# Kernel tuning notes

Measured on AMD Instinct MI355X. Metric: run time of the kernel, lower is better.

The kernel has to match this reference:

```python
import jax, jax.numpy as jnp
import numpy as np

NT, C, B, N, H, E = 32768, 128, 64, 512, 4, 524288  # total nodes, channels, graphs, nodes/graph, heads, edges
DH = C // H
EPS = 1e-5


def batchnorm(x, g, b):
    # BatchNorm1d over the node dimension (training-mode batch statistics)
    m = x.mean(axis=0)
    v = x.var(axis=0)
    return (x - m) * jax.lax.rsqrt(v + EPS) * g + b


def setup_inputs() -> dict:
    key = jax.random.key(0)
    ks = jax.random.split(key, 8)
    s = 1.0 / np.sqrt(C)
    return dict(
        x=jax.random.normal(ks[0], (NT, C), jnp.float32),
        edge_index=jax.random.randint(ks[1], (2, E), 0, NT, dtype=jnp.int32),
        Wc=jax.random.normal(ks[2], (C, C), jnp.float32) * s,
        bc=jnp.zeros((C,), jnp.float32),
        in_proj_w=jax.random.normal(ks[3], (3 * C, C), jnp.float32) * s,
        in_proj_b=jnp.zeros((3 * C,), jnp.float32),
        out_proj_w=jax.random.normal(ks[4], (C, C), jnp.float32) * s,
        out_proj_b=jnp.zeros((C,), jnp.float32),
        gn1=jnp.ones((C,), jnp.float32), bn1=jnp.zeros((C,), jnp.float32),
        gn2=jnp.ones((C,), jnp.float32), bn2=jnp.zeros((C,), jnp.float32),
        gn3=jnp.ones((C,), jnp.float32), bn3=jnp.zeros((C,), jnp.float32),
        Wm1=jax.random.normal(ks[5], (2 * C, C), jnp.float32) * s,
        bm1=jnp.zeros((2 * C,), jnp.float32),
        Wm2=jax.random.normal(ks[6], (C, 2 * C), jnp.float32) / np.sqrt(2 * C),
        bm2=jnp.zeros((C,), jnp.float32),
    )


def reference(x, edge_index, Wc, bc, in_proj_w, in_proj_b, out_proj_w, out_proj_b,
              gn1, bn1, gn2, bn2, gn3, bn3, Wm1, bm1, Wm2, bm2):
    # --- local branch: mean-aggregation message passing + linear + residual + BN ---
    src, dst = edge_index[0], edge_index[1]
    agg = jax.ops.segment_sum(x[src], dst, num_segments=NT)            # [NT, C]
    cnt = jax.ops.segment_sum(jnp.ones((E, 1), x.dtype), dst, num_segments=NT)
    agg = agg / jnp.maximum(cnt, 1.0)
    h_local = agg @ Wc.T + bc + x                                       # dropout p=0 -> no-op
    h_local = batchnorm(h_local, gn1, bn1)

    # --- global branch: to_dense_batch (equal-size graphs -> reshape) + MHA ---
    hd = x.reshape(B, N, C)
    qkv = hd @ in_proj_w.T + in_proj_b                                  # [B, N, 3C]
    q, k, v = jnp.split(qkv, 3, axis=-1)
    q = q.reshape(B, N, H, DH).transpose(0, 2, 1, 3)                    # [B, H, N, DH]
    k = k.reshape(B, N, H, DH).transpose(0, 2, 1, 3)
    v = v.reshape(B, N, H, DH).transpose(0, 2, 1, 3)
    scores = jnp.einsum('bhqd,bhkd->bhqk', q, k) / np.sqrt(DH)          # [B, H, N, N]
    attn = jax.nn.softmax(scores, axis=-1)
    o = jnp.einsum('bhqk,bhkd->bhqd', attn, v)                          # [B, H, N, DH]
    o = o.transpose(0, 2, 1, 3).reshape(B, N, C)
    h_attn = (o @ out_proj_w.T + out_proj_b).reshape(NT, C) + x
    h_attn = batchnorm(h_attn, gn2, bn2)

    # --- combine + MLP + final norm ---
    out = h_local + h_attn
    out = out + (jax.nn.relu(out @ Wm1.T + bm1) @ Wm2.T + bm2)
    return batchnorm(out, gn3, bn3)
```

## Files before the change

### kernel.cpp

```cpp
#include <hip/hip_runtime.h>
#include <cstddef>

#define NT    32768
#define CCH   128
#define BB    64
#define NNODE 512
#define NHEAD 4
#define DHEAD 32
#define EE    524288
#define EPS   1e-5f
#define MAXDEG 96
#define CURPAD 16
#define SSLOT  8
#define EGRP  2048

typedef unsigned short u16;
typedef unsigned int   u32;
typedef __attribute__((ext_vector_type(8))) short short8;
typedef __attribute__((ext_vector_type(4))) short short4v;
typedef __attribute__((ext_vector_type(4))) float f32x4;

__device__ __forceinline__ float b2f(u32 w) { return __uint_as_float(w << 16); }
__device__ __forceinline__ u16 f2b(float f) {
    u32 u = __float_as_uint(f);
    u += 0x7FFF + ((u >> 16) & 1);
    return (u16)(u >> 16);
}

__global__ __launch_bounds__(256) void prep_kernel(const float* __restrict__ x,
                                                   const float* __restrict__ Wc,
                                                   const float* __restrict__ Wqkv,
                                                   const float* __restrict__ Wo,
                                                   const float* __restrict__ Wm1,
                                                   const float* __restrict__ Wm2,
                                                   u16* __restrict__ xb,
                                                   u16* __restrict__ Wcb,
                                                   u16* __restrict__ Wqkvb,
                                                   u16* __restrict__ Wob,
                                                   u16* __restrict__ Wm1b,
                                                   u16* __restrict__ Wm2b,
                                                   const int* __restrict__ ei,
                                                   int* __restrict__ cursor,
                                                   int* __restrict__ bucket) {
    if (blockIdx.x >= 2120) {
        int b2 = blockIdx.x - 2120;
        int k = b2 & 7;
        int g = b2 >> 3;
        int base_e = g * EGRP;
        for (int j = threadIdx.x; j < EGRP; j += 256) {
            int dst = ei[EE + base_e + j];
            if ((dst & 7) == k) {
                int src = ei[base_e + j];
                int pos = atomicAdd(cursor + dst * CURPAD, 1);
                if (pos < MAXDEG) bucket[dst * MAXDEG + pos] = src;
            }
        }
        return;
    }
    int r = blockIdx.x * 256 + threadIdx.x;
    const float* src; u16* dst;
    if (r < 524288) { src = x; dst = xb; }
    else if ((r -= 524288) < 2048) { src = Wc; dst = Wcb; }
    else if ((r -= 2048) < 6144) { src = Wqkv; dst = Wqkvb; }
    else if ((r -= 6144) < 2048) { src = Wo; dst = Wob; }
    else if ((r -= 2048) < 4096) { src = Wm1; dst = Wm1b; }
    else { r -= 4096; src = Wm2; dst = Wm2b; }
    size_t base = (size_t)r * 8;
    float4 a = *(const float4*)(src + base);
    float4 b = *(const float4*)(src + base + 4);
    uint4 u;
    u.x = (u32)f2b(a.x) | ((u32)f2b(a.y) << 16);
    u.y = (u32)f2b(a.z) | ((u32)f2b(a.w) << 16);
    u.z = (u32)f2b(b.x) | ((u32)f2b(b.y) << 16);
    u.w = (u32)f2b(b.z) | ((u32)f2b(b.w) << 16);
    *(uint4*)(dst + base) = u;
}

__global__ __launch_bounds__(256) void aggregate(const int* __restrict__ bucket,
                                                 const int* __restrict__ cursor,
                                                 const u16* __restrict__ xb,
                                                 u16* __restrict__ agg) {
    __shared__ int srcs[16][MAXDEG];
    int ln = threadIdx.x >> 4;
    int c8 = threadIdx.x & 15;
    int n = blockIdx.x * 16 + ln;
    int d = min(cursor[n * CURPAD], MAXDEG);
    for (int j = c8; j < d; j += 16) srcs[ln][j] = bucket[n * MAXDEG + j];
    __syncthreads();
    const u16* xp = xb + c8 * 8;
    float s[8] = {0.f, 0.f, 0.f, 0.f, 0.f, 0.f, 0.f, 0.f};
    for (int base = 0; base < d; base += 8) {
        uint4 w[8];
#pragma unroll
        for (int u = 0; u < 8; ++u) {
            int jj = base + u;
            int idx = srcs[ln][jj < d ? jj : 0];
            w[u] = *(const uint4*)(xp + (size_t)idx * CCH);
        }
#pragma unroll
        for (int u = 0; u < 8; ++u) {
            if (base + u >= d) { w[u].x = 0; w[u].y = 0; w[u].z = 0; w[u].w = 0; }
            s[0] += b2f(w[u].x & 0xffffu);
            s[1] += b2f(w[u].x >> 16);
            s[2] += b2f(w[u].y & 0xffffu);
            s[3] += b2f(w[u].y >> 16);
            s[4] += b2f(w[u].z & 0xffffu);
            s[5] += b2f(w[u].z >> 16);
            s[6] += b2f(w[u].w & 0xffffu);
            s[7] += b2f(w[u].w >> 16);
        }
    }
    float inv = 1.0f / fmaxf((float)d, 1.0f);
    uint4 out;
    out.x = (u32)f2b(s[0] * inv) | ((u32)f2b(s[1] * inv) << 16);
    out.y = (u32)f2b(s[2] * inv) | ((u32)f2b(s[3] * inv) << 16);
    out.z = (u32)f2b(s[4] * inv) | ((u32)f2b(s[5] * inv) << 16);
    out.w = (u32)f2b(s[6] * inv) | ((u32)f2b(s[7] * inv) << 16);
    *(uint4*)(agg + (size_t)n * CCH + c8 * 8) = out;
}

struct GemmSmem {
    u16 As[128 * 32];
    u16 Bs[128 * 32];
    u16 Cs[4][16 * 72];
    float csum[128];
    float csq[128];
};

template <bool RELU, int RESID, bool STATS>
__device__ __forceinline__ void gemm_body(GemmSmem& sm,
                                          const u16* __restrict__ A,
                                          const u16* __restrict__ W,
                                          const float* __restrict__ bias,
                                          const u16* __restrict__ residb,
                                          u16* __restrict__ outb, int ostride,
                                          float* __restrict__ sum, float* __restrict__ sumsq,
                                          int slotbase, int m0, int K) {
    int tid = threadIdx.x;
    int lane = tid & 63, wave = tid >> 6;
    int wm = (wave & 1) * 64, wn = (wave >> 1) * 64;
    int l15 = lane & 15, l4 = lane >> 4;

    if (STATS) {
        if (tid < 128) { sm.csum[tid] = 0.f; sm.csq[tid] = 0.f; }
    }

    f32x4 zero = {0.f, 0.f, 0.f, 0.f};
    f32x4 acc[4][4];
#pragma unroll
    for (int i = 0; i < 4; ++i)
#pragma unroll
        for (int j = 0; j < 4; ++j) acc[i][j] = zero;

    int srow = tid >> 2;
    int scol = (tid & 3) * 8;

    int kIter = K >> 5;
    uint4 a0 = *(const uint4*)(A + (size_t)(m0 + srow) * K + scol);
    uint4 a1 = *(const uint4*)(A + (size_t)(m0 + srow + 64) * K + scol);
    uint4 b0 = *(const uint4*)(W + (size_t)srow * K + scol);
    uint4 b1 = *(const uint4*)(W + (size_t)(srow + 64) * K + scol);
    for (int ki = 0; ki < kIter; ++ki) {
        if (ki) __syncthreads();
        *(uint4*)&sm.As[srow * 32 + scol] = a0;
        *(uint4*)&sm.As[(srow + 64) * 32 + scol] = a1;
        *(uint4*)&sm.Bs[srow * 32 + scol] = b0;
        *(uint4*)&sm.Bs[(srow + 64) * 32 + scol] = b1;
        if (ki + 1 < kIter) {
            int k0 = (ki + 1) * 32;
            a0 = *(const uint4*)(A + (size_t)(m0 + srow) * K + k0 + scol);
            a1 = *(const uint4*)(A + (size_t)(m0 + srow + 64) * K + k0 + scol);
            b0 = *(const uint4*)(W + (size_t)srow * K + k0 + scol);
            b1 = *(const uint4*)(W + (size_t)(srow + 64) * K + k0 + scol);
        }
        __syncthreads();
        short8 af[4], bf[4];
#pragma unroll
        for (int t = 0; t < 4; ++t) {
            af[t] = *(const short8*)&sm.As[(wm + t * 16 + l15) * 32 + l4 * 8];
            bf[t] = *(const short8*)&sm.Bs[(wn + t * 16 + l15) * 32 + l4 * 8];
        }
#pragma unroll
        for (int mt = 0; mt < 4; ++mt)
#pragma unroll
            for (int nt = 0; nt < 4; ++nt)
                acc[mt][nt] = __builtin_amdgcn_mfma_f32_16x16x32_bf16(af[mt], bf[nt], acc[mt][nt], 0, 0, 0);
    }

    float ps[4] = {0.f, 0.f, 0.f, 0.f};
    float pq[4] = {0.f, 0.f, 0.f, 0.f};
    int rl = lane >> 3;
    int cg = lane & 7;
#pragma unroll
    for (int mt = 0; mt < 4; ++mt) {
#pragma unroll
        for (int nt = 0; nt < 4; ++nt) {
            int lcol = wn + nt * 16 + l15;
            float bs = bias[lcol];
#pragma unroll
            for (int r = 0; r < 4; ++r) {
                int row = m0 + wm + mt * 16 + l4 * 4 + r;
                float v = acc[mt][nt][r] + bs;
                if (RESID == 2) v += b2f(residb[(size_t)row * 128 + lcol]);
                if (RELU) v = fmaxf(v, 0.0f);
                sm.Cs[wave][(l4 * 4 + r) * 72 + nt * 16 + l15] = f2b(v);
                if (STATS) { ps[nt] += v; pq[nt] += v * v; }
            }
        }
#pragma unroll
        for (int p = 0; p < 2; ++p) {
            int lrow = p * 8 + rl;
            uint4 wv = *(const uint4*)&sm.Cs[wave][lrow * 72 + cg * 8];
            int grow = m0 + wm + mt * 16 + lrow;
            *(uint4*)(outb + (size_t)grow * ostride + wn + cg * 8) = wv;
        }
    }
    if (STATS) {
#pragma unroll
        for (int nt = 0; nt < 4; ++nt) {
            atomicAdd(&sm.csum[wn + nt * 16 + l15], ps[nt]);
            atomicAdd(&sm.csq[wn + nt * 16 + l15], pq[nt]);
        }
        __syncthreads();
        if (tid < 128) {
            atomicAdd(sum + slotbase + tid, sm.csum[tid]);
            atomicAdd(sumsq + slotbase + tid, sm.csq[tid]);
        }
    }
}

__global__ __launch_bounds__(256) void gemm_wc_qkv(const u16* __restrict__ aggb,
                                                   const u16* __restrict__ Wcb,
                                                   const float* __restrict__ bc,
                                                   const u16* __restrict__ xb,
                                                   u16* __restrict__ hlocb,
                                                   float* __restrict__ sum1,
                                                   float* __restrict__ sq1,
                                                   const u16* __restrict__ Wqkvb,
                                                   const float* __restrict__ bqkv,
                                                   u16* __restrict__ qkvb) {
    __shared__ GemmSmem sm;
    int y = blockIdx.y;
    int m0 = blockIdx.x * 128;
    if (y == 0) {
        gemm_body<false, 2, true>(sm, aggb, Wcb, bc, xb, hlocb, 128, sum1, sq1,
                                  (blockIdx.x & (SSLOT - 1)) << 7, m0, 128);
    } else {
        gemm_body<false, 0, false>(sm, xb, Wqkvb + (size_t)(y - 1) * 16384,
                                   bqkv + (y - 1) * 128, nullptr,
                                   qkvb + (y - 1) * 128, 384, nullptr, nullptr, 0, m0, 128);
    }
}

__global__ __launch_bounds__(256) void gemm_wo(const u16* __restrict__ ob,
                                               const u16* __restrict__ Wob,
                                               const float* __restrict__ bo,
                                               const u16* __restrict__ xb,
                                               u16* __restrict__ t2b,
                                               float* __restrict__ sum2, float* __restrict__ sq2) {
    __shared__ GemmSmem sm;
    gemm_body<false, 2, true>(sm, ob, Wob, bo, xb, t2b, 128, sum2, sq2,
                              (blockIdx.x & (SSLOT - 1)) << 7, blockIdx.x * 128, 128);
}

__global__ __launch_bounds__(256) void gemm_mlp2(const u16* __restrict__ hidb,
                                                 const u16* __restrict__ Wm2b,
                                                 const float* __restrict__ bm2,
                                                 const u16* __restrict__ shb,
                                                 u16* __restrict__ out2b,
                                                 float* __restrict__ sum3, float* __restrict__ sq3) {
    __shared__ GemmSmem sm;
    gemm_body<false, 2, true>(sm, hidb, Wm2b, bm2, shb, out2b, 128, sum3, sq3,
                              (blockIdx.x & (SSLOT - 1)) << 7, blockIdx.x * 128, 256);
}

__global__ __launch_bounds__(256) void gemm_m1c(const u16* __restrict__ hlocb,
                                                const u16* __restrict__ t2b,
                                                const float* __restrict__ sum1,
                                                const float* __restrict__ sq1,
                                                const float* __restrict__ g1,
                                                const float* __restrict__ bt1,
                                                const float* __restrict__ sum2,
                                                const float* __restrict__ sq2,
                                                const float* __restrict__ g2,
                                                const float* __restrict__ bt2,
                                                u16* __restrict__ shb,
                                                const u16* __restrict__ Wm1b,
                                                const float* __restrict__ bm1,
                                                u16* __restrict__ hidb) {
    __shared__ u16 As[128 * 32];
    __shared__ u16 Bs[128 * 32];
    __shared__ u16 Cs[4][16 * 72];
    __shared__ float AF1[128], BF1[128], AF2[128], BF2[128];
    int tid = threadIdx.x;
    {
        int c = tid & 127;
        const float* sm = (tid < 128) ? sum1 : sum2;
        const float* sq = (tid < 128) ? sq1 : sq2;
        const float* g  = (tid < 128) ? g1 : g2;
        const float* bt = (tid < 128) ? bt1 : bt2;
        float s = 0.f, q = 0.f;
#pragma unroll
        for (int sl = 0; sl < SSLOT; ++sl) { s += sm[sl * 128 + c]; q += sq[sl * 128 + c]; }
        float m = s * (1.0f / NT);
        float v = q * (1.0f / NT) - m * m;
        float a = g[c] * rsqrtf(v + EPS);
        if (tid < 128) { AF1[c] = a; BF1[c] = bt[c] - m * a; }
        else           { AF2[c] = a; BF2[c] = bt[c] - m * a; }
    }
    int m0 = blockIdx.x * 128, n0 = blockIdx.y * 128;
    int lane = tid & 63, wave = tid >> 6;
    int wm = (wave & 1) * 64, wn = (wave >> 1) * 64;
    int l15 = lane & 15, l4 = lane >> 4;

    f32x4 zero = {0.f, 0.f, 0.f, 0.f};
    f32x4 acc[4][4];
#pragma unroll
    for (int i = 0; i < 4; ++i)
#pragma unroll
        for (int j = 0; j < 4; ++j) acc[i][j] = zero;

    int srow = tid >> 2;
    int scol = (tid & 3) * 8;
    bool wr = (blockIdx.y == 0);

    uint4 h0 = *(const uint4*)(hlocb + (size_t)(m0 + srow) * 128 + scol);
    uint4 h1 = *(const uint4*)(hlocb + (size_t)(m0 + srow + 64) * 128 + scol);
    uint4 t0 = *(const uint4*)(t2b + (size_t)(m0 + srow) * 128 + scol);
    uint4 t1 = *(const uint4*)(t2b + (size_t)(m0 + srow + 64) * 128 + scol);
    uint4 b0 = *(const uint4*)(Wm1b + (size_t)(n0 + srow) * 128 + scol);
    uint4 b1 = *(const uint4*)(Wm1b + (size_t)(n0 + srow + 64) * 128 + scol);
    __syncthreads();
    for (int ki = 0; ki < 4; ++ki) {
        int k0 = ki * 32;
        if (ki) __syncthreads();
        uint4 c0, c1;
        {
            const u32 hw[4] = {h0.x, h0.y, h0.z, h0.w};
            const u32 tw[4] = {t0.x, t0.y, t0.z, t0.w};
            u32 ow[4];
#pragma unroll
            for (int p = 0; p < 4; ++p) {
                int cc = k0 + scol + p * 2;
                float v0 = AF1[cc] * b2f(hw[p] & 0xffffu) + BF1[cc] + AF2[cc] * b2f(tw[p] & 0xffffu) + BF2[cc];
                float v1 = AF1[cc + 1] * b2f(hw[p] >> 16) + BF1[cc + 1] + AF2[cc + 1] * b2f(tw[p] >> 16) + BF2[cc + 1];
                ow[p] = (u32)f2b(v0) | ((u32)f2b(v1) << 16);
            }
            c0.x = ow[0]; c0.y = ow[1]; c0.z = ow[2]; c0.w = ow[3];
        }
        {
            const u32 hw[4] = {h1.x, h1.y, h1.z, h1.w};
            const u32 tw[4] = {t1.x, t1.y, t1.z, t1.w};
            u32 ow[4];
#pragma unroll
            for (int p = 0; p < 4; ++p) {
                int cc = k0 + scol + p * 2;
                float v0 = AF1[cc] * b2f(hw[p] & 0xffffu) + BF1[cc] + AF2[cc] * b2f(tw[p] & 0xffffu) + BF2[cc];
                float v1 = AF1[cc + 1] * b2f(hw[p] >> 16) + BF1[cc + 1] + AF2[cc + 1] * b2f(tw[p] >> 16) + BF2[cc + 1];
                ow[p] = (u32)f2b(v0) | ((u32)f2b(v1) << 16);
            }
            c1.x = ow[0]; c1.y = ow[1]; c1.z = ow[2]; c1.w = ow[3];
        }
        *(uint4*)&As[srow * 32 + scol] = c0;
        *(uint4*)&As[(srow + 64) * 32 + scol] = c1;
        *(uint4*)&Bs[srow * 32 + scol] = b0;
        *(uint4*)&Bs[(srow + 64) * 32 + scol] = b1;
        if (wr) {
            *(uint4*)(shb + (size_t)(m0 + srow) * 128 + k0 + scol) = c0;
            *(uint4*)(shb + (size_t)(m0 + srow + 64) * 128 + k0 + scol) = c1;
        }
        if (ki < 3) {
            int kn = k0 + 32;
            h0 = *(const uint4*)(hlocb + (size_t)(m0 + srow) * 128 + kn + scol);
            h1 = *(const uint4*)(hlocb + (size_t)(m0 + srow + 64) * 128 + kn + scol);
            t0 = *(const uint4*)(t2b + (size_t)(m0 + srow) * 128 + kn + scol);
            t1 = *(const uint4*)(t2b + (size_t)(m0 + srow + 64) * 128 + kn + scol);
            b0 = *(const uint4*)(Wm1b + (size_t)(n0 + srow) * 128 + kn + scol);
            b1 = *(const uint4*)(Wm1b + (size_t)(n0 + srow + 64) * 128 + kn + scol);
        }
        __syncthreads();
        short8 af[4], bf[4];
#pragma unroll
        for (int t = 0; t < 4; ++t) {
            af[t] = *(const short8*)&As[(wm + t * 16 + l15) * 32 + l4 * 8];
            bf[t] = *(const short8*)&Bs[(wn + t * 16 + l15) * 32 + l4 * 8];
        }
#pragma unroll
        for (int mt = 0; mt < 4; ++mt)
#pragma unroll
            for (int nt = 0; nt < 4; ++nt)
                acc[mt][nt] = __builtin_amdgcn_mfma_f32_16x16x32_bf16(af[mt], bf[nt], acc[mt][nt], 0, 0, 0);
    }

    int rl = lane >> 3;
    int cg = lane & 7;
#pragma unroll
    for (int mt = 0; mt < 4; ++mt) {
#pragma unroll
        for (int nt = 0; nt < 4; ++nt) {
            int col = n0 + wn + nt * 16 + l15;
            float bs = bm1[col];
#pragma unroll
            for (int r = 0; r < 4; ++r) {
                float v = fmaxf(acc[mt][nt][r] + bs, 0.0f);
                Cs[wave][(l4 * 4 + r) * 72 + nt * 16 + l15] = f2b(v);
            }
        }
#pragma unroll
        for (int p = 0; p < 2; ++p) {
            int lrow = p * 8 + rl;
            uint4 wv = *(const uint4*)&Cs[wave][lrow * 72 + cg * 8];
            int grow = m0 + wm + mt * 16 + lrow;
            *(uint4*)(hidb + (size_t)grow * 256 + n0 + wn + cg * 8) = wv;
        }
    }
}

__global__ __launch_bounds__(256) void final_bn(const u16* __restrict__ X,
                                                const float* __restrict__ sum3,
                                                const float* __restrict__ sq3,
                                                const float* __restrict__ g3,
                                                const float* __restrict__ bt3,
                                                float* __restrict__ outp) {
    __shared__ float A3[128], B3[128];
    int t = threadIdx.x;
    if (t < 128) {
        float s = 0.f, q = 0.f;
#pragma unroll
        for (int sl = 0; sl < SSLOT; ++sl) { s += sum3[sl * 128 + t]; q += sq3[sl * 128 + t]; }
        float m = s * (1.0f / NT);
        float v = q * (1.0f / NT) - m * m;
        float a = g3[t] * rsqrtf(v + EPS);
        A3[t] = a;
        B3[t] = bt3[t] - m * a;
    }
    __syncthreads();
    int i8 = blockIdx.x * 256 + t;
    size_t i = (size_t)i8 * 8;
    int c = (int)(i & (CCH - 1));
    uint4 u = *(const uint4*)(X + i);
    float x[8];
    x[0] = b2f(u.x & 0xffffu); x[1] = b2f(u.x >> 16);
    x[2] = b2f(u.y & 0xffffu); x[3] = b2f(u.y >> 16);
    x[4] = b2f(u.z & 0xffffu); x[5] = b2f(u.z >> 16);
    x[6] = b2f(u.w & 0xffffu); x[7] = b2f(u.w >> 16);
    float4 o0, o1;
    o0.x = A3[c + 0] * x[0] + B3[c + 0];
    o0.y = A3[c + 1] * x[1] + B3[c + 1];
    o0.z = A3[c + 2] * x[2] + B3[c + 2];
    o0.w = A3[c + 3] * x[3] + B3[c + 3];
    o1.x = A3[c + 4] * x[4] + B3[c + 4];
    o1.y = A3[c + 5] * x[5] + B3[c + 5];
    o1.z = A3[c + 6] * x[6] + B3[c + 6];
    o1.w = A3[c + 7] * x[7] + B3[c + 7];
    *(float4*)(outp + i) = o0;
    *(float4*)(outp + i + 4) = o1;
}

__global__ __launch_bounds__(512) void attn_mfma(const u16* __restrict__ qkv,
                                                 u16* __restrict__ o) {
    __shared__ __align__(16) u16 Ks[512 * 40];
    __shared__ __align__(16) u16 Vt[32 * 520];
    int bh = blockIdx.x;
    int b = bh >> 2, h = bh & 3;
    int tid = threadIdx.x;
    int lane = tid & 63, wave = tid >> 6;
    int quad = lane >> 4, l15 = lane & 15;
    const float scale = 0.1767766952966369f;

    const u16* kvbase = qkv + (size_t)b * 512 * 384 + 128 + h * 32;
    for (int idx = tid; idx < 2048; idx += 512) {
        int row = idx >> 2, c = idx & 3;
        *(uint4*)&Ks[row * 40 + c * 8] = *(const uint4*)(kvbase + (size_t)row * 384 + c * 8);
    }
    for (int idx = tid; idx < 2048; idx += 512) {
        int row = idx >> 2, c = idx & 3;
        uint4 u = *(const uint4*)(kvbase + 128 + (size_t)row * 384 + c * 8);
        u16 e[8];
        *(uint4*)e = u;
#pragma unroll
        for (int i = 0; i < 8; ++i) Vt[(c * 8 + i) * 520 + row] = e[i];
    }
    __syncthreads();

    f32x4 zero = {0.f, 0.f, 0.f, 0.f};
    for (int qt = 0; qt < 4; ++qt) {
        int qbase = wave * 64 + qt * 16;
        short8 qf = *(const short8*)(qkv + (size_t)(b * 512 + qbase + l15) * 384 + h * 32 + quad * 8);
        float lq = 0.f;
        f32x4 oa[2] = {zero, zero};

        for (int kv0 = 0; kv0 < 512; kv0 += 64) {
            f32x4 s[4];
#pragma unroll
            for (int t = 0; t < 4; ++t) {
                short8 kb = *(const short8*)&Ks[(kv0 + t * 16 + l15) * 40 + quad * 8];
                s[t] = __builtin_amdgcn_mfma_f32_16x16x32_bf16(kb, qf, zero, 0, 0, 0);
            }
            short8 pp[2];
#pragma unroll
            for (int t = 0; t < 4; ++t) {
                float p0 = __expf(s[t][0] * scale);
                float p1 = __expf(s[t][1] * scale);
                float p2 = __expf(s[t][2] * scale);
                float p3 = __expf(s[t][3] * scale);
                lq += (p0 + p1) + (p2 + p3);
                int hi = (t & 1) * 4;
                pp[t >> 1][hi + 0] = (short)f2b(p0);
                pp[t >> 1][hi + 1] = (short)f2b(p1);
                pp[t >> 1][hi + 2] = (short)f2b(p2);
                pp[t >> 1][hi + 3] = (short)f2b(p3);
            }
#pragma unroll
            for (int tp = 0; tp < 2; ++tp) {
                int tb = kv0 + tp * 32;
#pragma unroll
                for (int n = 0; n < 2; ++n) {
                    const u16* vrow = &Vt[(n * 16 + l15) * 520 + tb + quad * 4];
                    short4v va = *(const short4v*)vrow;
                    short4v vb2 = *(const short4v*)(vrow + 16);
                    short8 vv = {va.x, va.y, va.z, va.w, vb2.x, vb2.y, vb2.z, vb2.w};
                    oa[n] = __builtin_amdgcn_mfma_f32_16x16x32_bf16(pp[tp], vv, oa[n], 0, 0, 0);
                }
            }
        }
        lq += __shfl_xor(lq, 16);
        lq += __shfl_xor(lq, 32);
        u16* op = o + (size_t)(b * 512 + qbase) * 128 + h * 32;
#pragma unroll
        for (int r = 0; r < 4; ++r) {
            float Lr = __shfl(lq, quad * 4 + r);
            float inv = 1.0f / Lr;
#pragma unroll
            for (int n = 0; n < 2; ++n)
                op[(quad * 4 + r) * 128 + n * 16 + l15] = f2b(oa[n][r] * inv);
        }
    }
}

extern "C" void kernel_launch(void* const* d_in, const int* in_sizes, int n_in,
                              void* d_out, int out_size, void* d_ws, size_t ws_size,
                              hipStream_t stream) {
    const float* x    = (const float*)d_in[0];
    const int*   ei   = (const int*)d_in[1];
    const float* Wc   = (const float*)d_in[2];
    const float* bc   = (const float*)d_in[3];
    const float* Wqkv = (const float*)d_in[4];
    const float* bqkv = (const float*)d_in[5];
    const float* Wo   = (const float*)d_in[6];
    const float* bo   = (const float*)d_in[7];
    const float* gn1  = (const float*)d_in[8];
    const float* bn1b = (const float*)d_in[9];
    const float* gn2  = (const float*)d_in[10];
    const float* bn2b = (const float*)d_in[11];
    const float* gn3  = (const float*)d_in[12];
    const float* bn3b = (const float*)d_in[13];
    const float* Wm1  = (const float*)d_in[14];
    const float* bm1  = (const float*)d_in[15];
    const float* Wm2  = (const float*)d_in[16];
    const float* bm2  = (const float*)d_in[17];
    float* outp = (float*)d_out;

    char* w = (char*)d_ws;
    const size_t MB = 1024 * 1024;
    u16* xb    = (u16*)(w);
    u16* hlocb = (u16*)(w + 8 * MB);
    u16* t2b   = (u16*)(w + 16 * MB);
    u16* out2b = (u16*)(w + 24 * MB);
    u16* qkvb  = (u16*)(w + 32 * MB);
    u16* hidb  = (u16*)(w + 56 * MB);
    u16* shb   = (u16*)(w + 72 * MB);
    int* bucket = (int*)(w + 80 * MB);
    int* cursor = (int*)(w + 92 * MB);
    float* stats = (float*)(w + 94 * MB);
    u16* Wcb   = (u16*)(w + 95 * MB);
    u16* Wqkvb = Wcb + 16384;
    u16* Wob   = Wqkvb + 49152;
    u16* Wm1b  = Wob + 16384;
    u16* Wm2b  = Wm1b + 32768;
    u16* ob    = (u16*)(w + 96 * MB);
    float* sum1 = stats;                  float* sq1 = stats + 1024;
    float* sum2 = stats + 2048;           float* sq2 = stats + 3072;
    float* sum3 = stats + 4096;           float* sq3 = stats + 5120;

    hipMemsetAsync(cursor, 0, 2 * MB + 6 * 1024 * 4, stream);

    prep_kernel<<<2120 + 2048, 256, 0, stream>>>(x, Wc, Wqkv, Wo, Wm1, Wm2,
                                                 xb, Wcb, Wqkvb, Wob, Wm1b, Wm2b,
                                                 ei, cursor, bucket);

    aggregate<<<NT / 16, 256, 0, stream>>>(bucket, cursor, xb, shb);

    {
        dim3 g(NT / 128, 4);
        gemm_wc_qkv<<<g, 256, 0, stream>>>(shb, Wcb, bc, xb, hlocb, sum1, sq1,
                                           Wqkvb, bqkv, qkvb);
    }

    attn_mfma<<<BB * NHEAD, 512, 0, stream>>>(qkvb, ob);

    gemm_wo<<<NT / 128, 256, 0, stream>>>(ob, Wob, bo, xb, t2b, sum2, sq2);

    {
        dim3 g(NT / 128, 2);
        gemm_m1c<<<g, 256, 0, stream>>>(hlocb, t2b, sum1, sq1, gn1, bn1b,
                                        sum2, sq2, gn2, bn2b, shb, Wm1b, bm1, hidb);
    }

    gemm_mlp2<<<NT / 128, 256, 0, stream>>>(hidb, Wm2b, bm2, shb, out2b, sum3, sq3);

    final_bn<<<NT * CCH / 8 / 256, 256, 0, stream>>>(out2b, sum3, sq3, gn3, bn3b, outp);
}
```

Baseline: 245.1 us.

## Fuse neighbor aggregation into the Wc GEMM block, keeping agg in shared memory

Removes the separate aggregate kernel. The y==0 blocks of gemm_wc_qkv now gather and average neighbor features for their 128 rows straight into a shared-memory A buffer laid out by K-slice, then run the Wc GEMM from shared memory. This drops one launch and the agg round trip through global memory. In exchange, the aggregation work is serialized into 256 blocks at 8 passes each, which lowers parallelism on the gather, and the larger shared-memory footprint may reduce occupancy for the QKV blocks.

```diff
diff --git a/kernel.cpp b/kernel.cpp
--- a/kernel.cpp
+++ b/kernel.cpp
@@ -76,49 +76,6 @@
     *(uint4*)(dst + base) = u;
 }
 
-__global__ __launch_bounds__(256) void aggregate(const int* __restrict__ bucket,
-                                                 const int* __restrict__ cursor,
-                                                 const u16* __restrict__ xb,
-                                                 u16* __restrict__ agg) {
-    __shared__ int srcs[16][MAXDEG];
-    int ln = threadIdx.x >> 4;
-    int c8 = threadIdx.x & 15;
-    int n = blockIdx.x * 16 + ln;
-    int d = min(cursor[n * CURPAD], MAXDEG);
-    for (int j = c8; j < d; j += 16) srcs[ln][j] = bucket[n * MAXDEG + j];
-    __syncthreads();
-    const u16* xp = xb + c8 * 8;
-    float s[8] = {0.f, 0.f, 0.f, 0.f, 0.f, 0.f, 0.f, 0.f};
-    for (int base = 0; base < d; base += 8) {
-        uint4 w[8];
-#pragma unroll
-        for (int u = 0; u < 8; ++u) {
-            int jj = base + u;
-            int idx = srcs[ln][jj < d ? jj : 0];
-            w[u] = *(const uint4*)(xp + (size_t)idx * CCH);
-        }
-#pragma unroll
-        for (int u = 0; u < 8; ++u) {
-            if (base + u >= d) { w[u].x = 0; w[u].y = 0; w[u].z = 0; w[u].w = 0; }
-            s[0] += b2f(w[u].x & 0xffffu);
-            s[1] += b2f(w[u].x >> 16);
-            s[2] += b2f(w[u].y & 0xffffu);
-            s[3] += b2f(w[u].y >> 16);
-            s[4] += b2f(w[u].z & 0xffffu);
-            s[5] += b2f(w[u].z >> 16);
-            s[6] += b2f(w[u].w & 0xffffu);
-            s[7] += b2f(w[u].w >> 16);
-        }
-    }
-    float inv = 1.0f / fmaxf((float)d, 1.0f);
-    uint4 out;
-    out.x = (u32)f2b(s[0] * inv) | ((u32)f2b(s[1] * inv) << 16);
-    out.y = (u32)f2b(s[2] * inv) | ((u32)f2b(s[3] * inv) << 16);
-    out.z = (u32)f2b(s[4] * inv) | ((u32)f2b(s[5] * inv) << 16);
-    out.w = (u32)f2b(s[6] * inv) | ((u32)f2b(s[7] * inv) << 16);
-    *(uint4*)(agg + (size_t)n * CCH + c8 * 8) = out;
-}
-
 struct GemmSmem {
     u16 As[128 * 32];
     u16 Bs[128 * 32];
@@ -127,8 +84,18 @@
     float csq[128];
 };
 
+struct FusedSmem {
+    u16 bufA[4][128 * 32];
+    u16 Bs[128 * 32];
+    u16 Cs[4][16 * 72];
+    float csum[128];
+    float csq[128];
+};
+
 template <bool RELU, int RESID, bool STATS>
-__device__ __forceinline__ void gemm_body(GemmSmem& sm,
+__device__ __forceinline__ void gemm_body(u16* __restrict__ As, u16* __restrict__ Bs,
+                                          u16* __restrict__ Cs0, float* __restrict__ csum,
+                                          float* __restrict__ csq,
                                           const u16* __restrict__ A,
                                           const u16* __restrict__ W,
                                           const float* __restrict__ bias,
@@ -140,9 +107,10 @@
     int lane = tid & 63, wave = tid >> 6;
     int wm = (wave & 1) * 64, wn = (wave >> 1) * 64;
     int l15 = lane & 15, l4 = lane >> 4;
+    u16* Csw = Cs0 + wave * (16 * 72);
 
     if (STATS) {
-        if (tid < 128) { sm.csum[tid] = 0.f; sm.csq[tid] = 0.f; }
+        if (tid < 128) { csum[tid] = 0.f; csq[tid] = 0.f; }
     }
 
     f32x4 zero = {0.f, 0.f, 0.f, 0.f};
@@ -162,10 +130,10 @@
     uint4 b1 = *(const uint4*)(W + (size_t)(srow + 64) * K + scol);
     for (int ki = 0; ki < kIter; ++ki) {
         if (ki) __syncthreads();
-        *(uint4*)&sm.As[srow * 32 + scol] = a0;
-        *(uint4*)&sm.As[(srow + 64) * 32 + scol] = a1;
-        *(uint4*)&sm.Bs[srow * 32 + scol] = b0;
-        *(uint4*)&sm.Bs[(srow + 64) * 32 + scol] = b1;
+        *(uint4*)&As[srow * 32 + scol] = a0;
+        *(uint4*)&As[(srow + 64) * 32 + scol] = a1;
+        *(uint4*)&Bs[srow * 32 + scol] = b0;
+        *(uint4*)&Bs[(srow + 64) * 32 + scol] = b1;
         if (ki + 1 < kIter) {
             int k0 = (ki + 1) * 32;
             a0 = *(const uint4*)(A + (size_t)(m0 + srow) * K + k0 + scol);
@@ -177,8 +145,8 @@
         short8 af[4], bf[4];
 #pragma unroll
         for (int t = 0; t < 4; ++t) {
-            af[t] = *(const short8*)&sm.As[(wm + t * 16 + l15) * 32 + l4 * 8];
-            bf[t] = *(const short8*)&sm.Bs[(wn + t * 16 + l15) * 32 + l4 * 8];
+            af[t] = *(const short8*)&As[(wm + t * 16 + l15) * 32 + l4 * 8];
+            bf[t] = *(const short8*)&Bs[(wn + t * 16 + l15) * 32 + l4 * 8];
         }
 #pragma unroll
         for (int mt = 0; mt < 4; ++mt)
@@ -203,14 +171,14 @@
                 float v = acc[mt][nt][r] + bs;
                 if (RESID == 2) v += b2f(residb[(size_t)row * 128 + lcol]);
                 if (RELU) v = fmaxf(v, 0.0f);
-                sm.Cs[wave][(l4 * 4 + r) * 72 + nt * 16 + l15] = f2b(v);
+                Csw[(l4 * 4 + r) * 72 + nt * 16 + l15] = f2b(v);
                 if (STATS) { ps[nt] += v; pq[nt] += v * v; }
             }
         }
 #pragma unroll
         for (int p = 0; p < 2; ++p) {
             int lrow = p * 8 + rl;
-            uint4 wv = *(const uint4*)&sm.Cs[wave][lrow * 72 + cg * 8];
+            uint4 wv = *(const uint4*)&Csw[lrow * 72 + cg * 8];
             int grow = m0 + wm + mt * 16 + lrow;
             *(uint4*)(outb + (size_t)grow * ostride + wn + cg * 8) = wv;
         }
@@ -218,18 +186,19 @@
     if (STATS) {
 #pragma unroll
         for (int nt = 0; nt < 4; ++nt) {
-            atomicAdd(&sm.csum[wn + nt * 16 + l15], ps[nt]);
-            atomicAdd(&sm.csq[wn + nt * 16 + l15], pq[nt]);
+            atomicAdd(&csum[wn + nt * 16 + l15], ps[nt]);
+            atomicAdd(&csq[wn + nt * 16 + l15], pq[nt]);
         }
         __syncthreads();
         if (tid < 128) {
-            atomicAdd(sum + slotbase + tid, sm.csum[tid]);
-            atomicAdd(sumsq + slotbase + tid, sm.csq[tid]);
-        }
-    }
-}
-
-__global__ __launch_bounds__(256) void gemm_wc_qkv(const u16* __restrict__ aggb,
+            atomicAdd(sum + slotbase + tid, csum[tid]);
+            atomicAdd(sumsq + slotbase + tid, csq[tid]);
+        }
+    }
+}
+
+__global__ __launch_bounds__(256) void gemm_wc_qkv(const int* __restrict__ bucket,
+                                                   const int* __restrict__ cursor,
                                                    const u16* __restrict__ Wcb,
                                                    const float* __restrict__ bc,
                                                    const u16* __restrict__ xb,
@@ -239,16 +208,141 @@
                                                    const u16* __restrict__ Wqkvb,
                                                    const float* __restrict__ bqkv,
                                                    u16* __restrict__ qkvb) {
-    __shared__ GemmSmem sm;
+    __shared__ FusedSmem sm;
     int y = blockIdx.y;
     int m0 = blockIdx.x * 128;
-    if (y == 0) {
-        gemm_body<false, 2, true>(sm, aggb, Wcb, bc, xb, hlocb, 128, sum1, sq1,
-                                  (blockIdx.x & (SSLOT - 1)) << 7, m0, 128);
-    } else {
-        gemm_body<false, 0, false>(sm, xb, Wqkvb + (size_t)(y - 1) * 16384,
+    int tid = threadIdx.x;
+
+    if (y != 0) {
+        gemm_body<false, 0, false>(&sm.bufA[0][0], sm.Bs, &sm.Cs[0][0], sm.csum, sm.csq,
+                                   xb, Wqkvb + (size_t)(y - 1) * 16384,
                                    bqkv + (y - 1) * 128, nullptr,
                                    qkvb + (y - 1) * 128, 384, nullptr, nullptr, 0, m0, 128);
+        return;
+    }
+
+    int (*srcs)[MAXDEG] = reinterpret_cast<int (*)[MAXDEG]>(&sm.Cs[0][0]);
+    int ln = tid >> 4;
+    int c8 = tid & 15;
+    for (int pass = 0; pass < 8; ++pass) {
+        int n = pass * 16 + ln;
+        int gn = m0 + n;
+        int d = min(cursor[gn * CURPAD], MAXDEG);
+        for (int j = c8; j < d; j += 16) srcs[ln][j] = bucket[gn * MAXDEG + j];
+        __syncthreads();
+        const u16* xp = xb + c8 * 8;
+        float s[8] = {0.f, 0.f, 0.f, 0.f, 0.f, 0.f, 0.f, 0.f};
+        for (int base = 0; base < d; base += 8) {
+            uint4 w[8];
+#pragma unroll
+            for (int u = 0; u < 8; ++u) {
+                int jj = base + u;
+                int idx = srcs[ln][jj < d ? jj : 0];
+                w[u] = *(const uint4*)(xp + (size_t)idx * CCH);
+            }
+#pragma unroll
+            for (int u = 0; u < 8; ++u) {
+                if (base + u >= d) { w[u].x = 0; w[u].y = 0; w[u].z = 0; w[u].w = 0; }
+                s[0] += b2f(w[u].x & 0xffffu);
+                s[1] += b2f(w[u].x >> 16);
+                s[2] += b2f(w[u].y & 0xffffu);
+                s[3] += b2f(w[u].y >> 16);
+                s[4] += b2f(w[u].z & 0xffffu);
+                s[5] += b2f(w[u].z >> 16);
+                s[6] += b2f(w[u].w & 0xffffu);
+                s[7] += b2f(w[u].w >> 16);
+            }
+        }
+        float inv = 1.0f / fmaxf((float)d, 1.0f);
+        uint4 out;
+        out.x = (u32)f2b(s[0] * inv) | ((u32)f2b(s[1] * inv) << 16);
+        out.y = (u32)f2b(s[2] * inv) | ((u32)f2b(s[3] * inv) << 16);
+        out.z = (u32)f2b(s[4] * inv) | ((u32)f2b(s[5] * inv) << 16);
+        out.w = (u32)f2b(s[6] * inv) | ((u32)f2b(s[7] * inv) << 16);
+        *(uint4*)&sm.bufA[c8 >> 2][n * 32 + (c8 & 3) * 8] = out;
+        __syncthreads();
+    }
+
+    {
+        int lane = tid & 63, wave = tid >> 6;
+        int wm = (wave & 1) * 64, wn = (wave >> 1) * 64;
+        int l15 = lane & 15, l4 = lane >> 4;
+        u16* Csw = &sm.Cs[0][0] + wave * (16 * 72);
+        if (tid < 128) { sm.csum[tid] = 0.f; sm.csq[tid] = 0.f; }
+
+        f32x4 zero = {0.f, 0.f, 0.f, 0.f};
+        f32x4 acc[4][4];
+#pragma unroll
+        for (int i = 0; i < 4; ++i)
+#pragma unroll
+            for (int j = 0; j < 4; ++j) acc[i][j] = zero;
+
+        int srow = tid >> 2;
+        int scol = (tid & 3) * 8;
+        uint4 b0 = *(const uint4*)(Wcb + (size_t)srow * 128 + scol);
+        uint4 b1 = *(const uint4*)(Wcb + (size_t)(srow + 64) * 128 + scol);
+        for (int ki = 0; ki < 4; ++ki) {
+            if (ki) __syncthreads();
+            *(uint4*)&sm.Bs[srow * 32 + scol] = b0;
+            *(uint4*)&sm.Bs[(srow + 64) * 32 + scol] = b1;
+            if (ki < 3) {
+                int k0 = (ki + 1) * 32;
+                b0 = *(const uint4*)(Wcb + (size_t)srow * 128 + k0 + scol);
+                b1 = *(const uint4*)(Wcb + (size_t)(srow + 64) * 128 + k0 + scol);
+            }
+            __syncthreads();
+            short8 af[4], bf[4];
+#pragma unroll
+            for (int t = 0; t < 4; ++t) {
+                af[t] = *(const short8*)&sm.bufA[ki][(wm + t * 16 + l15) * 32 + l4 * 8];
+                bf[t] = *(const short8*)&sm.Bs[(wn + t * 16 + l15) * 32 + l4 * 8];
+            }
+#pragma unroll
+            for (int mt = 0; mt < 4; ++mt)
+#pragma unroll
+                for (int nt = 0; nt < 4; ++nt)
+                    acc[mt][nt] = __builtin_amdgcn_mfma_f32_16x16x32_bf16(af[mt], bf[nt], acc[mt][nt], 0, 0, 0);
+        }
+        __syncthreads();
+
+        float ps[4] = {0.f, 0.f, 0.f, 0.f};
+        float pq[4] = {0.f, 0.f, 0.f, 0.f};
+        int rl = lane >> 3;
+        int cg = lane & 7;
+#pragma unroll
+        for (int mt = 0; mt < 4; ++mt) {
+#pragma unroll
+            for (int nt = 0; nt < 4; ++nt) {
+                int lcol = wn + nt * 16 + l15;
+                float bs = bc[lcol];
+#pragma unroll
+                for (int r = 0; r < 4; ++r) {
+                    int row = m0 + wm + mt * 16 + l4 * 4 + r;
+                    float v = acc[mt][nt][r] + bs;
+                    v += b2f(xb[(size_t)row * 128 + lcol]);
+                    Csw[(l4 * 4 + r) * 72 + nt * 16 + l15] = f2b(v);
+                    ps[nt] += v; pq[nt] += v * v;
+                }
+            }
+#pragma unroll
+            for (int p = 0; p < 2; ++p) {
+                int lrow = p * 8 + rl;
+                uint4 wv = *(const uint4*)&Csw[lrow * 72 + cg * 8];
+                int grow = m0 + wm + mt * 16 + lrow;
+                *(uint4*)(hlocb + (size_t)grow * 128 + cg * 8 + wn) = wv;
+            }
+        }
+#pragma unroll
+        for (int nt = 0; nt < 4; ++nt) {
+            atomicAdd(&sm.csum[wn + nt * 16 + l15], ps[nt]);
+            atomicAdd(&sm.csq[wn + nt * 16 + l15], pq[nt]);
+        }
+        __syncthreads();
+        if (tid < 128) {
+            int slotbase = (blockIdx.x & (SSLOT - 1)) << 7;
+            atomicAdd(sum1 + slotbase + tid, sm.csum[tid]);
+            atomicAdd(sq1 + slotbase + tid, sm.csq[tid]);
+        }
     }
 }
 
@@ -259,7 +353,8 @@
                                                u16* __restrict__ t2b,
                                                float* __restrict__ sum2, float* __restrict__ sq2) {
     __shared__ GemmSmem sm;
-    gemm_body<false, 2, true>(sm, ob, Wob, bo, xb, t2b, 128, sum2, sq2,
+    gemm_body<false, 2, true>(sm.As, sm.Bs, &sm.Cs[0][0], sm.csum, sm.csq,
+                              ob, Wob, bo, xb, t2b, 128, sum2, sq2,
                               (blockIdx.x & (SSLOT - 1)) << 7, blockIdx.x * 128, 128);
 }
 
@@ -270,7 +365,8 @@
                                                  u16* __restrict__ out2b,
                                                  float* __restrict__ sum3, float* __restrict__ sq3) {
     __shared__ GemmSmem sm;
-    gemm_body<false, 2, true>(sm, hidb, Wm2b, bm2, shb, out2b, 128, sum3, sq3,
+    gemm_body<false, 2, true>(sm.As, sm.Bs, &sm.Cs[0][0], sm.csum, sm.csq,
+                              hidb, Wm2b, bm2, shb, out2b, 128, sum3, sq3,
                               (blockIdx.x & (SSLOT - 1)) << 7, blockIdx.x * 128, 256);
 }
 
@@ -589,11 +685,9 @@
                                                  xb, Wcb, Wqkvb, Wob, Wm1b, Wm2b,
                                                  ei, cursor, bucket);
 
-    aggregate<<<NT / 16, 256, 0, stream>>>(bucket, cursor, xb, shb);
-
     {
         dim3 g(NT / 128, 4);
-        gemm_wc_qkv<<<g, 256, 0, stream>>>(shb, Wcb, bc, xb, hlocb, sum1, sq1,
+        gemm_wc_qkv<<<g, 256, 0, stream>>>(bucket, cursor, Wcb, bc, xb, hlocb, sum1, sq1,
                                            Wqkvb, bqkv, qkvb);
     }
 
```

Result: faster. 234.5 us (-4.3%).

## Fuse neighbor aggregation into the Wc/QKV GEMM kernel's local-branch blocks

Applied to the files above, without the earlier changes.

Removes the separate aggregate launch and has the y==0 blocks of gemm_wc_qkv gather and average neighbor features for their 128 rows, reusing shared memory for the source index lists, before running the Wc GEMM. This saves one kernel launch and lets the gather overlap with the QKV GEMM blocks running in the same grid. In exchange, the gather work is concentrated in 256 blocks that each do 8 serial passes with barriers, rather than spread across 2048 blocks, so those blocks become much longer and may load-imbalance the grid. The aggregate result still makes a round trip through global memory and is read back by the same block.

```diff
diff --git a/kernel.cpp b/kernel.cpp
--- a/kernel.cpp
+++ b/kernel.cpp
@@ -76,49 +76,6 @@
     *(uint4*)(dst + base) = u;
 }
 
-__global__ __launch_bounds__(256) void aggregate(const int* __restrict__ bucket,
-                                                 const int* __restrict__ cursor,
-                                                 const u16* __restrict__ xb,
-                                                 u16* __restrict__ agg) {
-    __shared__ int srcs[16][MAXDEG];
-    int ln = threadIdx.x >> 4;
-    int c8 = threadIdx.x & 15;
-    int n = blockIdx.x * 16 + ln;
-    int d = min(cursor[n * CURPAD], MAXDEG);
-    for (int j = c8; j < d; j += 16) srcs[ln][j] = bucket[n * MAXDEG + j];
-    __syncthreads();
-    const u16* xp = xb + c8 * 8;
-    float s[8] = {0.f, 0.f, 0.f, 0.f, 0.f, 0.f, 0.f, 0.f};
-    for (int base = 0; base < d; base += 8) {
-        uint4 w[8];
-#pragma unroll
-        for (int u = 0; u < 8; ++u) {
-            int jj = base + u;
-            int idx = srcs[ln][jj < d ? jj : 0];
-            w[u] = *(const uint4*)(xp + (size_t)idx * CCH);
-        }
-#pragma unroll
-        for (int u = 0; u < 8; ++u) {
-            if (base + u >= d) { w[u].x = 0; w[u].y = 0; w[u].z = 0; w[u].w = 0; }
-            s[0] += b2f(w[u].x & 0xffffu);
-            s[1] += b2f(w[u].x >> 16);
-            s[2] += b2f(w[u].y & 0xffffu);
-            s[3] += b2f(w[u].y >> 16);
-            s[4] += b2f(w[u].z & 0xffffu);
-            s[5] += b2f(w[u].z >> 16);
-            s[6] += b2f(w[u].w & 0xffffu);
-            s[7] += b2f(w[u].w >> 16);
-        }
-    }
-    float inv = 1.0f / fmaxf((float)d, 1.0f);
-    uint4 out;
-    out.x = (u32)f2b(s[0] * inv) | ((u32)f2b(s[1] * inv) << 16);
-    out.y = (u32)f2b(s[2] * inv) | ((u32)f2b(s[3] * inv) << 16);
-    out.z = (u32)f2b(s[4] * inv) | ((u32)f2b(s[5] * inv) << 16);
-    out.w = (u32)f2b(s[6] * inv) | ((u32)f2b(s[7] * inv) << 16);
-    *(uint4*)(agg + (size_t)n * CCH + c8 * 8) = out;
-}
-
 struct GemmSmem {
     u16 As[128 * 32];
     u16 Bs[128 * 32];
@@ -128,7 +85,9 @@
 };
 
 template <bool RELU, int RESID, bool STATS>
-__device__ __forceinline__ void gemm_body(GemmSmem& sm,
+__device__ __forceinline__ void gemm_body(u16* __restrict__ As, u16* __restrict__ Bs,
+                                          u16* __restrict__ Cs0, float* __restrict__ csum,
+                                          float* __restrict__ csq,
                                           const u16* __restrict__ A,
                                           const u16* __restrict__ W,
                                           const float* __restrict__ bias,
@@ -140,9 +99,10 @@
     int lane = tid & 63, wave = tid >> 6;
     int wm = (wave & 1) * 64, wn = (wave >> 1) * 64;
     int l15 = lane & 15, l4 = lane >> 4;
+    u16* Csw = Cs0 + wave * (16 * 72);
 
     if (STATS) {
-        if (tid < 128) { sm.csum[tid] = 0.f; sm.csq[tid] = 0.f; }
+        if (tid < 128) { csum[tid] = 0.f; csq[tid] = 0.f; }
     }
 
     f32x4 zero = {0.f, 0.f, 0.f, 0.f};
@@ -162,10 +122,10 @@
     uint4 b1 = *(const uint4*)(W + (size_t)(srow + 64) * K + scol);
     for (int ki = 0; ki < kIter; ++ki) {
         if (ki) __syncthreads();
-        *(uint4*)&sm.As[srow * 32 + scol] = a0;
-        *(uint4*)&sm.As[(srow + 64) * 32 + scol] = a1;
-        *(uint4*)&sm.Bs[srow * 32 + scol] = b0;
-        *(uint4*)&sm.Bs[(srow + 64) * 32 + scol] = b1;
+        *(uint4*)&As[srow * 32 + scol] = a0;
+        *(uint4*)&As[(srow + 64) * 32 + scol] = a1;
+        *(uint4*)&Bs[srow * 32 + scol] = b0;
+        *(uint4*)&Bs[(srow + 64) * 32 + scol] = b1;
         if (ki + 1 < kIter) {
             int k0 = (ki + 1) * 32;
             a0 = *(const uint4*)(A + (size_t)(m0 + srow) * K + k0 + scol);
@@ -177,8 +137,8 @@
         short8 af[4], bf[4];
 #pragma unroll
         for (int t = 0; t < 4; ++t) {
-            af[t] = *(const short8*)&sm.As[(wm + t * 16 + l15) * 32 + l4 * 8];
-            bf[t] = *(const short8*)&sm.Bs[(wn + t * 16 + l15) * 32 + l4 * 8];
+            af[t] = *(const short8*)&As[(wm + t * 16 + l15) * 32 + l4 * 8];
+            bf[t] = *(const short8*)&Bs[(wn + t * 16 + l15) * 32 + l4 * 8];
         }
 #pragma unroll
         for (int mt = 0; mt < 4; ++mt)
@@ -203,14 +163,14 @@
                 float v = acc[mt][nt][r] + bs;
                 if (RESID == 2) v += b2f(residb[(size_t)row * 128 + lcol]);
                 if (RELU) v = fmaxf(v, 0.0f);
-                sm.Cs[wave][(l4 * 4 + r) * 72 + nt * 16 + l15] = f2b(v);
+                Csw[(l4 * 4 + r) * 72 + nt * 16 + l15] = f2b(v);
                 if (STATS) { ps[nt] += v; pq[nt] += v * v; }
             }
         }
 #pragma unroll
         for (int p = 0; p < 2; ++p) {
             int lrow = p * 8 + rl;
-            uint4 wv = *(const uint4*)&sm.Cs[wave][lrow * 72 + cg * 8];
+            uint4 wv = *(const uint4*)&Csw[lrow * 72 + cg * 8];
             int grow = m0 + wm + mt * 16 + lrow;
             *(uint4*)(outb + (size_t)grow * ostride + wn + cg * 8) = wv;
         }
@@ -218,21 +178,23 @@
     if (STATS) {
 #pragma unroll
         for (int nt = 0; nt < 4; ++nt) {
-            atomicAdd(&sm.csum[wn + nt * 16 + l15], ps[nt]);
-            atomicAdd(&sm.csq[wn + nt * 16 + l15], pq[nt]);
+            atomicAdd(&csum[wn + nt * 16 + l15], ps[nt]);
+            atomicAdd(&csq[wn + nt * 16 + l15], pq[nt]);
         }
         __syncthreads();
         if (tid < 128) {
-            atomicAdd(sum + slotbase + tid, sm.csum[tid]);
-            atomicAdd(sumsq + slotbase + tid, sm.csq[tid]);
-        }
-    }
-}
-
-__global__ __launch_bounds__(256) void gemm_wc_qkv(const u16* __restrict__ aggb,
+            atomicAdd(sum + slotbase + tid, csum[tid]);
+            atomicAdd(sumsq + slotbase + tid, csq[tid]);
+        }
+    }
+}
+
+__global__ __launch_bounds__(256) void gemm_wc_qkv(const int* __restrict__ bucket,
+                                                   const int* __restrict__ cursor,
                                                    const u16* __restrict__ Wcb,
                                                    const float* __restrict__ bc,
                                                    const u16* __restrict__ xb,
+                                                   u16* __restrict__ aggb,
                                                    u16* __restrict__ hlocb,
                                                    float* __restrict__ sum1,
                                                    float* __restrict__ sq1,
@@ -242,14 +204,64 @@
     __shared__ GemmSmem sm;
     int y = blockIdx.y;
     int m0 = blockIdx.x * 128;
-    if (y == 0) {
-        gemm_body<false, 2, true>(sm, aggb, Wcb, bc, xb, hlocb, 128, sum1, sq1,
-                                  (blockIdx.x & (SSLOT - 1)) << 7, m0, 128);
-    } else {
-        gemm_body<false, 0, false>(sm, xb, Wqkvb + (size_t)(y - 1) * 16384,
+    int tid = threadIdx.x;
+
+    if (y != 0) {
+        gemm_body<false, 0, false>(sm.As, sm.Bs, &sm.Cs[0][0], sm.csum, sm.csq,
+                                   xb, Wqkvb + (size_t)(y - 1) * 16384,
                                    bqkv + (y - 1) * 128, nullptr,
                                    qkvb + (y - 1) * 128, 384, nullptr, nullptr, 0, m0, 128);
-    }
+        return;
+    }
+
+    {
+        int (*srcs)[MAXDEG] = reinterpret_cast<int (*)[MAXDEG]>(sm.As);
+        int ln = tid >> 4;
+        int c8 = tid & 15;
+        const u16* xp = xb + c8 * 8;
+        for (int pass = 0; pass < 8; ++pass) {
+            int n = pass * 16 + ln;
+            int gn = m0 + n;
+            int d = min(cursor[gn * CURPAD], MAXDEG);
+            for (int j = c8; j < d; j += 16) srcs[ln][j] = bucket[gn * MAXDEG + j];
+            __syncthreads();
+            float s[8] = {0.f, 0.f, 0.f, 0.f, 0.f, 0.f, 0.f, 0.f};
+            for (int base = 0; base < d; base += 8) {
+                uint4 w[8];
+#pragma unroll
+                for (int u = 0; u < 8; ++u) {
+                    int jj = base + u;
+                    int idx = srcs[ln][jj < d ? jj : 0];
+                    w[u] = *(const uint4*)(xp + (size_t)idx * CCH);
+                }
+#pragma unroll
+                for (int u = 0; u < 8; ++u) {
+                    if (base + u >= d) { w[u].x = 0; w[u].y = 0; w[u].z = 0; w[u].w = 0; }
+                    s[0] += b2f(w[u].x & 0xffffu);
+                    s[1] += b2f(w[u].x >> 16);
+                    s[2] += b2f(w[u].y & 0xffffu);
+                    s[3] += b2f(w[u].y >> 16);
+                    s[4] += b2f(w[u].z & 0xffffu);
+                    s[5] += b2f(w[u].z >> 16);
+                    s[6] += b2f(w[u].w & 0xffffu);
+                    s[7] += b2f(w[u].w >> 16);
+                }
+            }
+            float inv = 1.0f / fmaxf((float)d, 1.0f);
+            uint4 out;
+            out.x = (u32)f2b(s[0] * inv) | ((u32)f2b(s[1] * inv) << 16);
+            out.y = (u32)f2b(s[2] * inv) | ((u32)f2b(s[3] * inv) << 16);
+            out.z = (u32)f2b(s[4] * inv) | ((u32)f2b(s[5] * inv) << 16);
+            out.w = (u32)f2b(s[6] * inv) | ((u32)f2b(s[7] * inv) << 16);
+            *(uint4*)(aggb + (size_t)gn * CCH + c8 * 8) = out;
+            __syncthreads();
+        }
+    }
+    __syncthreads();
+
+    gemm_body<false, 2, true>(sm.As, sm.Bs, &sm.Cs[0][0], sm.csum, sm.csq,
+                              aggb, Wcb, bc, xb, hlocb, 128, sum1, sq1,
+                              (blockIdx.x & (SSLOT - 1)) << 7, m0, 128);
 }
 
 __global__ __launch_bounds__(256) void gemm_wo(const u16* __restrict__ ob,
@@ -259,7 +271,8 @@
                                                u16* __restrict__ t2b,
                                                float* __restrict__ sum2, float* __restrict__ sq2) {
     __shared__ GemmSmem sm;
-    gemm_body<false, 2, true>(sm, ob, Wob, bo, xb, t2b, 128, sum2, sq2,
+    gemm_body<false, 2, true>(sm.As, sm.Bs, &sm.Cs[0][0], sm.csum, sm.csq,
+                              ob, Wob, bo, xb, t2b, 128, sum2, sq2,
                               (blockIdx.x & (SSLOT - 1)) << 7, blockIdx.x * 128, 128);
 }
 
@@ -270,7 +283,8 @@
                                                  u16* __restrict__ out2b,
                                                  float* __restrict__ sum3, float* __restrict__ sq3) {
     __shared__ GemmSmem sm;
-    gemm_body<false, 2, true>(sm, hidb, Wm2b, bm2, shb, out2b, 128, sum3, sq3,
+    gemm_body<false, 2, true>(sm.As, sm.Bs, &sm.Cs[0][0], sm.csum, sm.csq,
+                              hidb, Wm2b, bm2, shb, out2b, 128, sum3, sq3,
                               (blockIdx.x & (SSLOT - 1)) << 7, blockIdx.x * 128, 256);
 }
 
@@ -589,11 +603,9 @@
                                                  xb, Wcb, Wqkvb, Wob, Wm1b, Wm2b,
                                                  ei, cursor, bucket);
 
-    aggregate<<<NT / 16, 256, 0, stream>>>(bucket, cursor, xb, shb);
-
     {
         dim3 g(NT / 128, 4);
-        gemm_wc_qkv<<<g, 256, 0, stream>>>(shb, Wcb, bc, xb, hlocb, sum1, sq1,
+        gemm_wc_qkv<<<g, 256, 0, stream>>>(bucket, cursor, Wcb, bc, xb, shb, hlocb, sum1, sq1,
                                            Wqkvb, bqkv, qkvb);
     }
 
```

Result: faster. 232.7 us (-5.1%).
